# Optimization experiments

Hardware: AMD Instinct MI355X
Metric: run time of the kernel (lower is better)

Reference implementation:

```python
import jax, jax.numpy as jnp
import numpy as np

N = 9
CELLS = N * N  # 81
B = 1024
HID = 100
EMPTY_P = 0.3


def _build_constraint_mask():
    # (81, 3, 81): mask[q, g, k] = 1 if cell k is in the same row/col/box as cell q
    m = np.zeros((CELLS, 3, CELLS), np.float32)
    for q in range(CELLS):
        r, c = divmod(q, N)
        for k in range(CELLS):
            r2, c2 = divmod(k, N)
            if r2 == r:
                m[q, 0, k] = 1.0
            if c2 == c:
                m[q, 1, k] = 1.0
            if (r2 // 3 == r // 3) and (c2 // 3 == c // 3):
                m[q, 2, k] = 1.0
    return jnp.asarray(m)


def setup_inputs() -> dict:
    key = jax.random.key(0)
    k1, k2, k3, k4 = jax.random.split(key, 4)
    # partially-filled boards: one-hot digits, ~EMPTY_P of cells zeroed (empty)
    digits = jax.random.randint(k1, (B, CELLS), 0, N)
    onehot = jax.nn.one_hot(digits, N, dtype=jnp.float32)
    filled = (jax.random.uniform(k2, (B, CELLS)) > EMPTY_P).astype(jnp.float32)
    x = onehot * filled[..., None]
    W1 = jax.random.normal(k3, (HID, 3 * N), dtype=jnp.float32) * 0.1
    W2 = jax.random.normal(k4, (N, HID), dtype=jnp.float32) * 0.1
    c = _build_constraint_mask()
    return {"x": x, "c": c, "W1": W1, "W2": W2}


def reference(x, c, W1, W2):
    bts = x.shape[0]
    # min_empty: max number of empty cells over the batch (fixed loop count, as in torch)
    T = int(jnp.max(jnp.sum(x.sum(axis=2) == 0, axis=1)))
    bidx = jnp.arange(bts)

    def step(carry, _):
        xc, xp = carry
        # constraints[b,q,g,d] = sum_k xc[b,k,d] * c[q,g,k]  (sparse graph aggregation)
        cons = jnp.einsum('bkd,qgk->bqgd', xc, c).reshape(bts, CELLS, 3 * N)
        empty = xc.sum(axis=2) == 0  # (B, 81)
        # masked MLP: compute everywhere, use only where empty (same math)
        y = jax.nn.relu(cons @ W1.T) @ W2.T  # (B, 81, 9)
        s_ = jax.nn.softmax(y, axis=-1)
        xp = jnp.where(empty[..., None], s_, xp)
        s = jnp.where(empty[..., None], s_, 0.0)
        score = s.max(axis=2)           # (B, 81)
        score_pos = s.argmax(axis=2)    # (B, 81)
        mmax = score.argmax(axis=1)     # (B,) most confident empty cell per board
        digit = score_pos[bidx, mmax]   # (B,)
        new_x = xc.at[bidx, mmax, digit].set(1.0)
        has_empty = empty.any(axis=1)
        xc = jnp.where(has_empty[:, None, None], new_x, xc)
        return (xc, xp), None

    (x_final, x_pred), _ = jax.lax.scan(step, (x, x), None, length=T)
    return (x_pred, x_final)
```

## Files before the change

### kernel.cpp

```cpp
#include <hip/hip_runtime.h>

#define CELLS 81
#define ND 9
#define HID 100
#define NP 52
#define PPW 13
#define NREG 8

typedef float v2f __attribute__((ext_vector_type(2)));

#define W1P_SZ (9 * NP * 8)
#define W2P_SZ (NP * 20)
#define NE_OFF (W1P_SZ + W2P_SZ)
#define ORD_OFF (NE_OFF + 1024)

__global__ __launch_bounds__(64) void prep_ne_kernel(
    const float* __restrict__ x_all,
    const float* __restrict__ W1, const float* __restrict__ W2,
    float* __restrict__ ws, int* __restrict__ ne, int* __restrict__ order,
    int nBoards)
{
    const int b = blockIdx.x, t = threadIdx.x;

    if (t < 2) order[2 * b + t] = -1;

    const float* xb = x_all + (size_t)b * (CELLS * ND);
    float mx = 0.f;
    #pragma unroll
    for (int d = 0; d < ND; ++d) mx = fmaxf(mx, xb[t*ND + d]);
    bool e1 = (mx < 0.5f);
    bool e2 = false;
    if (t < CELLS - 64) {
        float m2 = 0.f;
        #pragma unroll
        for (int d = 0; d < ND; ++d) m2 = fmaxf(m2, xb[(64+t)*ND + d]);
        e2 = (m2 < 0.5f);
    }
    unsigned long long m1 = __ballot(e1), m2b = __ballot(e2);
    if (t == 0) ne[b] = __popcll(m1) + __popcll(m2b);

    if (b == 0) {
        for (int i = t; i < 9 * NP; i += 64) {
            int d = i / NP, j = i - d * NP;
            float* r = ws + (size_t)i * 8;
            if (j < 50) {
                int u0 = 2 * j, u1 = u0 + 1;
                r[0] = W1[u0*27 + d];      r[1] = W1[u1*27 + d];
                r[2] = W1[u0*27 + 9 + d];  r[3] = W1[u1*27 + 9 + d];
                r[4] = W1[u0*27 + 18 + d]; r[5] = W1[u1*27 + 18 + d];
            } else {
                r[0]=r[1]=r[2]=r[3]=r[4]=r[5]=0.f;
            }
            r[6] = 0.f; r[7] = 0.f;
        }
        for (int j = t; j < NP; j += 64) {
            float* r = ws + W1P_SZ + (size_t)j * 20;
            if (j < 50) {
                int u0 = 2 * j, u1 = u0 + 1;
                #pragma unroll
                for (int d = 0; d < ND; ++d) {
                    r[2*d]     = W2[d*HID + u0];
                    r[2*d + 1] = W2[d*HID + u1];
                }
            } else {
                #pragma unroll
                for (int d = 0; d < ND; ++d) { r[2*d] = 0.f; r[2*d+1] = 0.f; }
            }
            r[18] = 0.f; r[19] = 0.f;
        }
    }
}

__global__ __launch_bounds__(64) void part_kernel(
    const int* __restrict__ ne, int* __restrict__ order, int nBoards)
{
    __shared__ int s_ne[1024];
    const int t0 = threadIdx.x;
    const int t  = blockIdx.x * 64 + t0;
    for (int j = t0; j < 1024; j += 64)
        s_ne[j] = (j < nBoards) ? ne[j] : -1;
    __syncthreads();
    const int key = (t < nBoards) ? s_ne[t] : -2;
    int pos = 0, nBig = 0;
    #pragma unroll 8
    for (int j = 0; j < 1024; ++j) {
        int kj = s_ne[j];
        pos  += (kj > key) || (kj == key && j < t);
        nBig += (kj > 32);
    }
    if (t < nBoards) {
        if (key > 32) {
            order[2*pos] = t; order[2*pos + 1] = t;
        } else {
            int r = pos - nBig;
            int bb = nBig + (r >> 1);
            order[2*bb + (r & 1)] = t;
        }
    }
}

__global__ __launch_bounds__(256, 2) void sudoku_kernel(
    const float* __restrict__ x_all,
    const float* __restrict__ ws,
    const int* __restrict__ order,
    float* __restrict__ out, int nBoards)
{
    const int tid = threadIdx.x;
    const int wv  = tid >> 6;
    const int lw  = tid & 63;
    const int h   = lw >> 5;
    const int jbase = wv * PPW;

    const int s0  = order[2 * blockIdx.x];
    const int s1r = order[2 * blockIdx.x + 1];
    if (s0 < 0) return;
    const int s1 = (s1r < 0) ? s0 : s1r;
    const bool joined = (s0 == s1);
    const int myBoard = h ? s1 : s0;
    const int idx = joined ? 0 : h;

    float* pom = out + (size_t)myBoard * (CELLS * ND);

    __shared__ __align__(16) float w1s[W1P_SZ];
    __shared__ __align__(16) float w2s[W2P_SZ];
    __shared__ float parts[2][4][ND][64];
    __shared__ float cnt[2][3 * 81];
    __shared__ int   digit[2][CELLS];

    for (int i = tid; i < W1P_SZ / 4; i += 256)
        ((float4*)w1s)[i] = ((const float4*)ws)[i];
    for (int i = tid; i < W2P_SZ / 4; i += 256)
        ((float4*)w2s)[i] = ((const float4*)(ws + W1P_SZ))[i];
    for (int i = tid; i < 2 * 243; i += 256) (&cnt[0][0])[i] = 0.f;
    __syncthreads();

    float w2reg[NREG][18];
    #pragma unroll
    for (int j = 0; j < NREG; ++j) {
        const float* qq = &w2s[(jbase + j) * 20];
        #pragma unroll
        for (int k = 0; k < 18; ++k) w2reg[j][k] = qq[k];
    }

    {
        const int slot = (tid < 128) ? 0 : 1;
        const int t = (tid < 128) ? tid : tid - 128;
        const bool doSlot = (slot == 0) || !joined;
        const int bd = slot ? s1 : s0;
        const float* xb = x_all + (size_t)bd * (CELLS * ND);
        float* pob = out + (size_t)bd * (CELLS * ND);
        if (doSlot) {
            if (t < CELLS) {
                int dig = -1;
                #pragma unroll
                for (int d = 0; d < ND; ++d)
                    if (dig < 0 && xb[t*ND + d] > 0.5f) dig = d;
                digit[slot][t] = dig;
                if (dig >= 0) {
                    int r = t/9, c = t%9, b = (r/3)*3 + c/3;
                    atomicAdd(&cnt[slot][r*9 + dig], 1.f);
                    atomicAdd(&cnt[slot][81 + c*9 + dig], 1.f);
                    atomicAdd(&cnt[slot][162 + b*9 + dig], 1.f);
                }
            }
            for (int i = t; i < CELLS * ND; i += 128) pob[i] = xb[i];
        }
    }
    __syncthreads();

    const int rank = joined ? lw : (lw & 31);
    int myq = 127;
    int ne0 = 0, ne1 = 0;
    for (int q = 0; q < CELLS; ++q)
        if (digit[0][q] < 0) { if (idx == 0 && ne0 == rank) myq = q; ++ne0; }
    if (!joined) {
        for (int q = 0; q < CELLS; ++q)
            if (digit[1][q] < 0) { if (idx == 1 && ne1 == rank) myq = q; ++ne1; }
    } else ne1 = ne0;
    if (ne0 > 64) ne0 = 64;
    if (ne1 > 64) ne1 = 64;
    const int ne_mine = idx ? ne1 : ne0;
    const int itMax = max(ne0, ne1);
    bool active = (rank < ne_mine);

    const int myr = (myq < 81) ? myq / 9 : 0;
    const int myc = (myq < 81) ? myq % 9 : 0;
    const int myb = (myr / 3) * 3 + myc / 3;

    float crr[9], ccc[9], cbb[9];
    #pragma unroll
    for (int j = 0; j < 9; ++j) {
        crr[j] = cnt[idx][myr*9 + j];
        ccc[j] = cnt[idx][81 + myc*9 + j];
        cbb[j] = cnt[idx][162 + myb*9 + j];
    }
    v2f z2[PPW];
    #pragma unroll
    for (int j = 0; j < PPW; ++j) {
        v2f a = (v2f){0.f, 0.f};
        #pragma unroll
        for (int d = 0; d < 9; ++d) {
            const float* p = &w1s[(d*NP + jbase + j) * 8];
            float4 ab = *(const float4*)p;
            v2f Cv = *(const v2f*)(p + 4);
            v2f Av = (v2f){ab.x, ab.y}, Bv = (v2f){ab.z, ab.w};
            a += crr[d]*Av + ccc[d]*Bv + cbb[d]*Cv;
        }
        z2[j] = a;
    }

    int dc = 0;
    v2f b0v = (v2f){0.f,0.f}, b1v = (v2f){0.f,0.f}, b2v = (v2f){0.f,0.f};
    float pfin[ND];

    for (int it = 0; it < itMax; ++it) {
        const float* w1r = &w1s[(dc*NP + jbase) * 8];
        const float* w2r = &w2s[jbase * 20];

        v2f acc2[ND];
        #pragma unroll
        for (int d = 0; d < ND; ++d) acc2[d] = (v2f){0.f, 0.f};

        #pragma unroll
        for (int j = 0; j < PPW; ++j) {
            const float* p = w1r + j*8;
            float4 ab = *(const float4*)p;
            v2f Cv = *(const v2f*)(p + 4);
            v2f Av = (v2f){ab.x, ab.y}, Bv = (v2f){ab.z, ab.w};
            v2f zv = z2[j];
            zv = b0v*Av + (b1v*Bv + (b2v*Cv + zv));
            z2[j] = zv;
            v2f hh;
            hh.x = fmaxf(zv.x, 0.f);
            hh.y = fmaxf(zv.y, 0.f);
            if (j < NREG) {
                #pragma unroll
                for (int d = 0; d < ND; ++d)
                    acc2[d] += hh * (v2f){w2reg[j][2*d], w2reg[j][2*d + 1]};
            } else {
                const float* qq = w2r + j*20;
                float4 w01 = *(const float4*)qq;
                float4 w23 = *(const float4*)(qq + 4);
                float4 w45 = *(const float4*)(qq + 8);
                float4 w67 = *(const float4*)(qq + 12);
                v2f w8 = *(const v2f*)(qq + 16);
                acc2[0] += hh * (v2f){w01.x, w01.y};
                acc2[1] += hh * (v2f){w01.z, w01.w};
                acc2[2] += hh * (v2f){w23.x, w23.y};
                acc2[3] += hh * (v2f){w23.z, w23.w};
                acc2[4] += hh * (v2f){w45.x, w45.y};
                acc2[5] += hh * (v2f){w45.z, w45.w};
                acc2[6] += hh * (v2f){w67.x, w67.y};
                acc2[7] += hh * (v2f){w67.z, w67.w};
                acc2[8] += hh * w8;
            }
        }

        const int buf = it & 1;
        #pragma unroll
        for (int d = 0; d < ND; ++d)
            parts[buf][wv][d][lw] = acc2[d].x + acc2[d].y;
        __syncthreads();

        float acc[ND];
        #pragma unroll
        for (int d = 0; d < ND; ++d) acc[d] = parts[buf][0][d][lw];
        #pragma unroll
        for (int ow = 1; ow < 4; ++ow) {
            #pragma unroll
            for (int d = 0; d < ND; ++d) acc[d] += parts[buf][ow][d][lw];
        }

        float m9 = fmaxf(fmaxf(fmaxf(acc[0],acc[1]), fmaxf(acc[2],acc[3])),
                         fmaxf(fmaxf(acc[4],acc[5]), fmaxf(acc[6],acc[7])));
        m9 = fmaxf(m9, acc[8]);
        float s = 0.f;
        #pragma unroll
        for (int d = 0; d < ND; ++d) { acc[d] = __expf(acc[d] - m9); s += acc[d]; }
        float inv = 1.f / s;
        float bv = -1.f; int bd = 0;
        #pragma unroll
        for (int d = 0; d < ND; ++d) {
            acc[d] *= inv;
            if (acc[d] > bv) { bv = acc[d]; bd = d; }
        }

        float bvv = active ? bv : -1.f;
        float vmax = bvv;
        #pragma unroll
        for (int off = 16; off >= 1; off >>= 1)
            vmax = fmaxf(vmax, __shfl_xor(vmax, off));
        if (joined) vmax = fmaxf(vmax, __shfl_xor(vmax, 32));
        const unsigned long long segMask =
            joined ? ~0ull : (h ? 0xFFFFFFFF00000000ull : 0x00000000FFFFFFFFull);
        unsigned long long msk = __ballot(active && (bvv == vmax)) & segMask;
        const bool valid = (msk != 0);
        int wl = valid ? (__ffsll(msk) - 1) : 0;
        int qw = __shfl(myq, wl);
        int dwn = __shfl(bd, wl);

        if (active && valid && myq == qw) {
            #pragma unroll
            for (int d = 0; d < ND; ++d) pfin[d] = acc[d];
            if (wv == 0) digit[idx][myq] = dwn;
            active = false;
        }
        const int pr = qw/9, pcc = qw%9, pb = (pr/3)*3 + pcc/3;
        b0v = (v2f)((valid && myr == pr)  ? 1.f : 0.f);
        b1v = (v2f)((valid && myc == pcc) ? 1.f : 0.f);
        b2v = (v2f)((valid && myb == pb)  ? 1.f : 0.f);
        if (valid) dc = dwn;
    }

    __syncthreads();
    if (wv == 0 && myq < 81) {
        #pragma unroll
        for (int d = 0; d < ND; ++d) pom[myq*ND + d] = pfin[d];
    }
    {
        const int slot = (tid < 128) ? 0 : 1;
        const int t = (tid < 128) ? tid : tid - 128;
        const bool doSlot = (slot == 0) || !joined;
        const int bd2 = slot ? s1 : s0;
        float* fob = out + (size_t)nBoards * (CELLS * ND) + (size_t)bd2 * (CELLS * ND);
        if (doSlot) {
            for (int i = t; i < CELLS * ND; i += 128) {
                int q = i / ND, d = i - q * ND;
                fob[i] = (digit[slot][q] == d) ? 1.f : 0.f;
            }
        }
    }
}

extern "C" void kernel_launch(void* const* d_in, const int* in_sizes, int n_in,
                              void* d_out, int out_size, void* d_ws, size_t ws_size,
                              hipStream_t stream) {
    const float* x  = (const float*)d_in[0];
    const float* W1 = (const float*)d_in[2];
    const float* W2 = (const float*)d_in[3];
    float* out = (float*)d_out;
    float* ws  = (float*)d_ws;
    int nBoards = in_sizes[0] / (CELLS * ND);
    int* neArr  = (int*)ws + NE_OFF;
    int* ordArr = (int*)ws + ORD_OFF;
    prep_ne_kernel<<<nBoards, 64, 0, stream>>>(x, W1, W2, ws, neArr, ordArr, nBoards);
    int partBlocks = (nBoards + 63) / 64;
    part_kernel<<<partBlocks, 64, 0, stream>>>(neArr, ordArr, nBoards);
    sudoku_kernel<<<nBoards, 256, 0, stream>>>(x, ws, ordArr, out, nBoards);
}
```

Baseline: 140.5 us.

## Precompute combined W1 delta table and replace sort with atomic bucketing

Result: slower. 157.1 us (+11.8%).

```diff
diff --git a/kernel.cpp b/kernel.cpp
--- a/kernel.cpp
+++ b/kernel.cpp
@@ -9,20 +9,62 @@
 
 typedef float v2f __attribute__((ext_vector_type(2)));
 
+#define TROW 106
+#define T_SZ (9 * 8 * TROW)
+#define W1P_OFF T_SZ
 #define W1P_SZ (9 * NP * 8)
+#define W2P_OFF (W1P_OFF + W1P_SZ)
 #define W2P_SZ (NP * 20)
-#define NE_OFF (W1P_SZ + W2P_SZ)
-#define ORD_OFF (NE_OFF + 1024)
-
-__global__ __launch_bounds__(64) void prep_ne_kernel(
+#define CNT_OFF (W2P_OFF + W2P_SZ)
+#define ORD_OFF (CNT_OFF + 4)
+#define BIGSLOTS 64
+#define SPILLSLOTS 8
+#define NBLK (BIGSLOTS + 512 + SPILLSLOTS)
+
+__global__ __launch_bounds__(64) void prep_kernel(
     const float* __restrict__ x_all,
     const float* __restrict__ W1, const float* __restrict__ W2,
-    float* __restrict__ ws, int* __restrict__ ne, int* __restrict__ order,
+    float* __restrict__ ws, int* __restrict__ cnts, int* __restrict__ order,
     int nBoards)
 {
     const int b = blockIdx.x, t = threadIdx.x;
-
-    if (t < 2) order[2 * b + t] = -1;
+    const int gid = b * 64 + t;
+
+    if (gid < T_SZ) {
+        int row = gid / TROW, off = gid - row * TROW;
+        float v = 0.f;
+        if (off < 104) {
+            int pair = off >> 1, u = 2 * pair + (off & 1);
+            if (pair < 50) {
+                int dc = row >> 3, m = row & 7;
+                if (m & 1) v += W1[u*27 + dc];
+                if (m & 2) v += W1[u*27 + 9 + dc];
+                if (m & 4) v += W1[u*27 + 18 + dc];
+            }
+        }
+        ws[gid] = v;
+    } else if (gid < W2P_OFF) {
+        int f = gid - W1P_OFF;
+        int i = f >> 3, k = f & 7;
+        int d = i / NP, j = i - d * NP;
+        float v = 0.f;
+        if (j < 50 && k < 6) {
+            int u = 2 * j + (k & 1);
+            v = W1[u*27 + (k >> 1) * 9 + d];
+        }
+        ws[gid] = v;
+    } else if (gid < CNT_OFF) {
+        int f = gid - W2P_OFF;
+        int j = f / 20, k = f - j * 20;
+        float v = 0.f;
+        if (j < 50 && k < 18) {
+            int d = k >> 1, u = 2 * j + (k & 1);
+            v = W2[d*HID + u];
+        }
+        ws[gid] = v;
+    }
+
+    if (b >= nBoards) return;
 
     const float* xb = x_all + (size_t)b * (CELLS * ND);
     float mx = 0.f;
@@ -37,64 +79,16 @@
         e2 = (m2 < 0.5f);
     }
     unsigned long long m1 = __ballot(e1), m2b = __ballot(e2);
-    if (t == 0) ne[b] = __popcll(m1) + __popcll(m2b);
-
-    if (b == 0) {
-        for (int i = t; i < 9 * NP; i += 64) {
-            int d = i / NP, j = i - d * NP;
-            float* r = ws + (size_t)i * 8;
-            if (j < 50) {
-                int u0 = 2 * j, u1 = u0 + 1;
-                r[0] = W1[u0*27 + d];      r[1] = W1[u1*27 + d];
-                r[2] = W1[u0*27 + 9 + d];  r[3] = W1[u1*27 + 9 + d];
-                r[4] = W1[u0*27 + 18 + d]; r[5] = W1[u1*27 + 18 + d];
-            } else {
-                r[0]=r[1]=r[2]=r[3]=r[4]=r[5]=0.f;
-            }
-            r[6] = 0.f; r[7] = 0.f;
-        }
-        for (int j = t; j < NP; j += 64) {
-            float* r = ws + W1P_SZ + (size_t)j * 20;
-            if (j < 50) {
-                int u0 = 2 * j, u1 = u0 + 1;
-                #pragma unroll
-                for (int d = 0; d < ND; ++d) {
-                    r[2*d]     = W2[d*HID + u0];
-                    r[2*d + 1] = W2[d*HID + u1];
-                }
-            } else {
-                #pragma unroll
-                for (int d = 0; d < ND; ++d) { r[2*d] = 0.f; r[2*d+1] = 0.f; }
-            }
-            r[18] = 0.f; r[19] = 0.f;
-        }
-    }
-}
-
-__global__ __launch_bounds__(64) void part_kernel(
-    const int* __restrict__ ne, int* __restrict__ order, int nBoards)
-{
-    __shared__ int s_ne[1024];
-    const int t0 = threadIdx.x;
-    const int t  = blockIdx.x * 64 + t0;
-    for (int j = t0; j < 1024; j += 64)
-        s_ne[j] = (j < nBoards) ? ne[j] : -1;
-    __syncthreads();
-    const int key = (t < nBoards) ? s_ne[t] : -2;
-    int pos = 0, nBig = 0;
-    #pragma unroll 8
-    for (int j = 0; j < 1024; ++j) {
-        int kj = s_ne[j];
-        pos  += (kj > key) || (kj == key && j < t);
-        nBig += (kj > 32);
-    }
-    if (t < nBoards) {
-        if (key > 32) {
-            order[2*pos] = t; order[2*pos + 1] = t;
+    if (t == 0) {
+        int ne = __popcll(m1) + __popcll(m2b);
+        if (ne > 32) {
+            int p = atomicAdd(&cnts[0], 1);
+            int blk = (p < BIGSLOTS) ? p : (BIGSLOTS + 512 + (p - BIGSLOTS));
+            if (blk < NBLK) { order[2*blk] = b; order[2*blk + 1] = b; }
         } else {
-            int r = pos - nBig;
-            int bb = nBig + (r >> 1);
-            order[2*bb + (r & 1)] = t;
+            int p = atomicAdd(&cnts[1], 1);
+            int blk = BIGSLOTS + (p >> 1);
+            order[2*blk + (p & 1)] = b;
         }
     }
 }
@@ -121,25 +115,25 @@
 
     float* pom = out + (size_t)myBoard * (CELLS * ND);
 
-    __shared__ __align__(16) float w1s[W1P_SZ];
+    __shared__ __align__(16) float tS[T_SZ];
     __shared__ __align__(16) float w2s[W2P_SZ];
-    __shared__ float parts[2][4][ND][64];
+    __shared__ v2f parts[2][4][5][64];
     __shared__ float cnt[2][3 * 81];
     __shared__ int   digit[2][CELLS];
 
-    for (int i = tid; i < W1P_SZ / 4; i += 256)
-        ((float4*)w1s)[i] = ((const float4*)ws)[i];
+    for (int i = tid; i < T_SZ / 4; i += 256)
+        ((float4*)tS)[i] = ((const float4*)ws)[i];
     for (int i = tid; i < W2P_SZ / 4; i += 256)
-        ((float4*)w2s)[i] = ((const float4*)(ws + W1P_SZ))[i];
+        ((float4*)w2s)[i] = ((const float4*)(ws + W2P_OFF))[i];
     for (int i = tid; i < 2 * 243; i += 256) (&cnt[0][0])[i] = 0.f;
     __syncthreads();
 
+    const float* w2g = ws + W2P_OFF;
     float w2reg[NREG][18];
     #pragma unroll
     for (int j = 0; j < NREG; ++j) {
-        const float* qq = &w2s[(jbase + j) * 20];
-        #pragma unroll
-        for (int k = 0; k < 18; ++k) w2reg[j][k] = qq[k];
+        #pragma unroll
+        for (int k = 0; k < 18; ++k) w2reg[j][k] = w2g[(jbase + j) * 20 + k];
     }
 
     {
@@ -194,13 +188,14 @@
         ccc[j] = cnt[idx][81 + myc*9 + j];
         cbb[j] = cnt[idx][162 + myb*9 + j];
     }
+    const float* w1g = ws + W1P_OFF;
     v2f z2[PPW];
     #pragma unroll
     for (int j = 0; j < PPW; ++j) {
         v2f a = (v2f){0.f, 0.f};
         #pragma unroll
         for (int d = 0; d < 9; ++d) {
-            const float* p = &w1s[(d*NP + jbase + j) * 8];
+            const float* p = &w1g[(d*NP + jbase + j) * 8];
             float4 ab = *(const float4*)p;
             v2f Cv = *(const v2f*)(p + 4);
             v2f Av = (v2f){ab.x, ab.y}, Bv = (v2f){ab.z, ab.w};
@@ -209,13 +204,11 @@
         z2[j] = a;
     }
 
-    int dc = 0;
-    v2f b0v = (v2f){0.f,0.f}, b1v = (v2f){0.f,0.f}, b2v = (v2f){0.f,0.f};
+    int dc = 0, mym = 0;
     float pfin[ND];
 
     for (int it = 0; it < itMax; ++it) {
-        const float* w1r = &w1s[(dc*NP + jbase) * 8];
-        const float* w2r = &w2s[jbase * 20];
+        const float* tT = &tS[(dc*8 + mym) * TROW + jbase*2];
 
         v2f acc2[ND];
         #pragma unroll
@@ -223,12 +216,8 @@
 
         #pragma unroll
         for (int j = 0; j < PPW; ++j) {
-            const float* p = w1r + j*8;
-            float4 ab = *(const float4*)p;
-            v2f Cv = *(const v2f*)(p + 4);
-            v2f Av = (v2f){ab.x, ab.y}, Bv = (v2f){ab.z, ab.w};
-            v2f zv = z2[j];
-            zv = b0v*Av + (b1v*Bv + (b2v*Cv + zv));
+            v2f dz = *(const v2f*)&tT[j*2];
+            v2f zv = z2[j] + dz;
             z2[j] = zv;
             v2f hh;
             hh.x = fmaxf(zv.x, 0.f);
@@ -238,7 +227,7 @@
                 for (int d = 0; d < ND; ++d)
                     acc2[d] += hh * (v2f){w2reg[j][2*d], w2reg[j][2*d + 1]};
             } else {
-                const float* qq = w2r + j*20;
+                const float* qq = &w2s[(jbase + j) * 20];
                 float4 w01 = *(const float4*)qq;
                 float4 w23 = *(const float4*)(qq + 4);
                 float4 w45 = *(const float4*)(qq + 8);
@@ -256,19 +245,24 @@
             }
         }
 
+        float accH[10];
+        #pragma unroll
+        for (int d = 0; d < ND; ++d) accH[d] = acc2[d].x + acc2[d].y;
+        accH[9] = 0.f;
         const int buf = it & 1;
         #pragma unroll
-        for (int d = 0; d < ND; ++d)
-            parts[buf][wv][d][lw] = acc2[d].x + acc2[d].y;
+        for (int k = 0; k < 5; ++k)
+            parts[buf][wv][k][lw] = (v2f){accH[2*k], accH[2*k + 1]};
         __syncthreads();
 
         float acc[ND];
         #pragma unroll
-        for (int d = 0; d < ND; ++d) acc[d] = parts[buf][0][d][lw];
-        #pragma unroll
-        for (int ow = 1; ow < 4; ++ow) {
+        for (int k = 0; k < 5; ++k) {
+            v2f s = parts[buf][0][k][lw];
             #pragma unroll
-            for (int d = 0; d < ND; ++d) acc[d] += parts[buf][ow][d][lw];
+            for (int ow = 1; ow < 4; ++ow) s += parts[buf][ow][k][lw];
+            acc[2*k] = s.x;
+            if (k < 4) acc[2*k + 1] = s.y;
         }
 
         float m9 = fmaxf(fmaxf(fmaxf(acc[0],acc[1]), fmaxf(acc[2],acc[3])),
@@ -306,9 +300,8 @@
             active = false;
         }
         const int pr = qw/9, pcc = qw%9, pb = (pr/3)*3 + pcc/3;
-        b0v = (v2f)((valid && myr == pr)  ? 1.f : 0.f);
-        b1v = (v2f)((valid && myc == pcc) ? 1.f : 0.f);
-        b2v = (v2f)((valid && myb == pb)  ? 1.f : 0.f);
+        mym = valid ? (((myr == pr) ? 1 : 0) | ((myc == pcc) ? 2 : 0)
+                     | ((myb == pb) ? 4 : 0)) : 0;
         if (valid) dc = dwn;
     }
 
@@ -341,10 +334,11 @@
     float* out = (float*)d_out;
     float* ws  = (float*)d_ws;
     int nBoards = in_sizes[0] / (CELLS * ND);
-    int* neArr  = (int*)ws + NE_OFF;
+    int* cnts   = (int*)ws + CNT_OFF;
     int* ordArr = (int*)ws + ORD_OFF;
-    prep_ne_kernel<<<nBoards, 64, 0, stream>>>(x, W1, W2, ws, neArr, ordArr, nBoards);
-    int partBlocks = (nBoards + 63) / 64;
-    part_kernel<<<partBlocks, 64, 0, stream>>>(neArr, ordArr, nBoards);
-    sudoku_kernel<<<nBoards, 256, 0, stream>>>(x, ws, ordArr, out, nBoards);
+    hipMemsetAsync(cnts, 0, 2 * sizeof(int), stream);
+    hipMemsetAsync(ordArr, 0xFF, 2 * NBLK * sizeof(int), stream);
+    int prepBlocks = (nBoards > 194) ? nBoards : 194;
+    prep_kernel<<<prepBlocks, 64, 0, stream>>>(x, W1, W2, ws, cnts, ordArr, nBoards);
+    sudoku_kernel<<<NBLK, 256, 0, stream>>>(x, ws, ordArr, out, nBoards);
 }
```
